# Kernel tuning notes

Measured on AMD Instinct MI355X. Metric: run time of the kernel, lower is better.

## Reference

```python
import jax, jax.numpy as jnp
import numpy as np

D_MODEL = 1024
D_HIDDEN = 32   # per-head MPS bond dimension
N_HEADS = 8
D_FF = 4096
EPS_LN = 1e-5
EPS_NORM = 1e-6


def layernorm(x, g, b):
    m = jnp.mean(x, axis=-1, keepdims=True)
    v = jnp.mean(jnp.square(x - m), axis=-1, keepdims=True)
    return (x - m) * jax.lax.rsqrt(v + EPS_LN) * g + b


def mps_recurrence(x, Wa, ba, h0, Wo, bo):
    # x: [B,S,D]. Per-token per-head transfer matrices A_t in R^{dh x dh}.
    B, S, D = x.shape
    A = (x @ Wa + ba).reshape(B, S, N_HEADS, D_HIDDEN, D_HIDDEN)
    A = jnp.moveaxis(A, 1, 0)  # [S,B,H,dh,dh]
    h_init = jnp.broadcast_to(h0, (B, N_HEADS, D_HIDDEN))  # [B,H,dh]

    def step(h, A_t):
        h = jnp.einsum('bhij,bhj->bhi', A_t, h)
        h = h / (jnp.linalg.norm(h, axis=-1, keepdims=True) + EPS_NORM)
        return h, h

    _, ys = jax.lax.scan(step, h_init, A)          # ys: [S,B,H,dh]
    ys = jnp.moveaxis(ys, 0, 1).reshape(B, S, N_HEADS * D_HIDDEN)
    return ys @ Wo + bo                            # [B,S,D]


def setup_inputs() -> dict:
    key = jax.random.key(0)
    ks = jax.random.split(key, 12)
    B, S, D = 4, 2048, D_MODEL
    inv = 1.0 / np.sqrt(D)
    inv_hd = 1.0 / np.sqrt(N_HEADS * D_HIDDEN)
    return {
        'x': jax.random.normal(ks[0], (B, S, D), jnp.float32),
        'ln1_g': jnp.ones((D,), jnp.float32),
        'ln1_b': jnp.zeros((D,), jnp.float32),
        'Wa': jax.random.normal(ks[1], (D, N_HEADS * D_HIDDEN * D_HIDDEN), jnp.float32) * inv,
        'ba': jnp.zeros((N_HEADS * D_HIDDEN * D_HIDDEN,), jnp.float32),
        'h0': jax.random.normal(ks[2], (N_HEADS, D_HIDDEN), jnp.float32) / np.sqrt(D_HIDDEN),
        'Wo': jax.random.normal(ks[3], (N_HEADS * D_HIDDEN, D), jnp.float32) * inv_hd,
        'bo': jnp.zeros((D,), jnp.float32),
        'ln2_g': jnp.ones((D,), jnp.float32),
        'ln2_b': jnp.zeros((D,), jnp.float32),
        'W1': jax.random.normal(ks[4], (D, D_FF), jnp.float32) * inv,
        'b1': jnp.zeros((D_FF,), jnp.float32),
        'W2': jax.random.normal(ks[5], (D_FF, D), jnp.float32) / np.sqrt(D_FF),
        'b2': jnp.zeros((D,), jnp.float32),
    }


def reference(x, ln1_g, ln1_b, Wa, ba, h0, Wo, bo, ln2_g, ln2_b, W1, b1, W2, b2):
    # Dropout in eval mode (identity).
    x = x + mps_recurrence(layernorm(x, ln1_g, ln1_b), Wa, ba, h0, Wo, bo)
    h = layernorm(x, ln2_g, ln2_b)
    ffn = jax.nn.gelu(h @ W1 + b1, approximate=False) @ W2 + b2
    return x + ffn
```

## Files before the change

### kernel.cpp

```cpp
#include <hip/hip_runtime.h>
#include <hip/hip_bf16.h>
#include <math.h>

typedef float f32x4 __attribute__((ext_vector_type(4)));
typedef __bf16 bf16x4 __attribute__((ext_vector_type(4)));
typedef __bf16 bf16x8 __attribute__((ext_vector_type(8)));

#define AS1(p) ((const __attribute__((address_space(1))) void*)(p))
#define AS3(p) ((__attribute__((address_space(3))) void*)(p))

static constexpr int D_MODEL = 1024;
static constexpr int S_LEN   = 2048;
static constexpr int BATCH   = 4;
static constexpr int NTOK    = BATCH * S_LEN;
static constexpr int NH      = 8;
static constexpr int DH      = 32;
static constexpr int NA      = NH * DH * DH;
static constexpr int D_FF    = 4096;
static constexpr int CHUNK   = 16;
static constexpr int NCHUNK  = S_LEN / CHUNK;

__device__ __forceinline__ void xcd_swizzle(int& bx, int& by) {
  int gx = gridDim.x;
  int nwg = gx * gridDim.y;
  int bid = by * gx + bx;
  int swz = (bid & 7) * (nwg >> 3) + (bid >> 3);
  bx = swz % gx;
  by = swz / gx;
}

__device__ __forceinline__ float gelu_erf_fast(float v) {
  float z = fabsf(v) * 0.70710678118654752f;
  float t = __builtin_amdgcn_rcpf(fmaf(0.3275911f, z, 1.0f));
  float p = t * (0.254829592f + t * (-0.284496736f + t * (1.421413741f +
            t * (-1.453152027f + t * 1.061405429f))));
  float e = __builtin_amdgcn_exp2f(-1.4426950408889634f * z * z);
  float er = 1.0f - p * e;
  er = (v < 0.0f) ? -er : er;
  return 0.5f * v * (1.0f + er);
}

__global__ __launch_bounds__(256) void transpose_bf16(
    const float* __restrict__ in, __bf16* __restrict__ out, int R, int C) {
  __shared__ float tile[32][33];
  int tx = threadIdx.x & 31, ty = threadIdx.x >> 5;
  int c0 = blockIdx.x * 32, r0 = blockIdx.y * 32;
  for (int i = ty; i < 32; i += 8)
    tile[i][tx] = in[(size_t)(r0 + i) * C + c0 + tx];
  __syncthreads();
  for (int i = ty; i < 32; i += 8)
    out[(size_t)(c0 + i) * R + r0 + tx] = (__bf16)tile[tx][i];
}

__global__ __launch_bounds__(256) void transpose_split(
    const float* __restrict__ in, __bf16* __restrict__ ohi,
    __bf16* __restrict__ olo, int R, int C) {
  __shared__ float tile[32][33];
  int tx = threadIdx.x & 31, ty = threadIdx.x >> 5;
  int c0 = blockIdx.x * 32, r0 = blockIdx.y * 32;
  for (int i = ty; i < 32; i += 8)
    tile[i][tx] = in[(size_t)(r0 + i) * C + c0 + tx];
  __syncthreads();
  for (int i = ty; i < 32; i += 8) {
    float v = tile[tx][i];
    __bf16 h = (__bf16)v;
    ohi[(size_t)(c0 + i) * R + r0 + tx] = h;
    olo[(size_t)(c0 + i) * R + r0 + tx] = (__bf16)(v - (float)h);
  }
}

template <int MODE>
__global__ __launch_bounds__(256) void ln_kernel(
    const float* __restrict__ in, const float* __restrict__ g,
    const float* __restrict__ bta, void* __restrict__ outv,
    void* __restrict__ outv2) {
  int row = blockIdx.x, tid = threadIdx.x;
  const float4* in4 = (const float4*)(in + (size_t)row * D_MODEL);
  float4 v = in4[tid];
  float s  = v.x + v.y + v.z + v.w;
  float ss = v.x * v.x + v.y * v.y + v.z * v.z + v.w * v.w;
  for (int o = 32; o; o >>= 1) { s += __shfl_down(s, o); ss += __shfl_down(ss, o); }
  __shared__ float ps[4], pq[4];
  int lane = tid & 63, w = tid >> 6;
  if (lane == 0) { ps[w] = s; pq[w] = ss; }
  __syncthreads();
  s  = ps[0] + ps[1] + ps[2] + ps[3];
  ss = pq[0] + pq[1] + pq[2] + pq[3];
  float mean = s * (1.0f / D_MODEL);
  float var  = ss * (1.0f / D_MODEL) - mean * mean;
  float inv  = rsqrtf(fmaxf(var, 0.0f) + 1e-5f);
  float4 gv = ((const float4*)g)[tid];
  float4 bv = ((const float4*)bta)[tid];
  float o0 = (v.x - mean) * inv * gv.x + bv.x;
  float o1 = (v.y - mean) * inv * gv.y + bv.y;
  float o2 = (v.z - mean) * inv * gv.z + bv.z;
  float o3 = (v.w - mean) * inv * gv.w + bv.w;
  if (MODE == 1) {
    float4 o = {o0, o1, o2, o3};
    ((float4*)outv)[(size_t)row * (D_MODEL / 4) + tid] = o;
  } else if (MODE == 0) {
    bf16x4 o;
    o[0] = (__bf16)o0; o[1] = (__bf16)o1; o[2] = (__bf16)o2; o[3] = (__bf16)o3;
    ((bf16x4*)outv)[(size_t)row * (D_MODEL / 4) + tid] = o;
  } else {
    bf16x4 oh, ol;
    oh[0] = (__bf16)o0; oh[1] = (__bf16)o1; oh[2] = (__bf16)o2; oh[3] = (__bf16)o3;
    ol[0] = (__bf16)(o0 - (float)oh[0]);
    ol[1] = (__bf16)(o1 - (float)oh[1]);
    ol[2] = (__bf16)(o2 - (float)oh[2]);
    ol[3] = (__bf16)(o3 - (float)oh[3]);
    ((bf16x4*)outv )[(size_t)row * (D_MODEL / 4) + tid] = oh;
    ((bf16x4*)outv2)[(size_t)row * (D_MODEL / 4) + tid] = ol;
  }
}

__global__ __launch_bounds__(256) void gemm_split_f32out(
    const __bf16* __restrict__ Ahi, const __bf16* __restrict__ Alo,
    const __bf16* __restrict__ BThi, const __bf16* __restrict__ BTlo,
    const float* __restrict__ bias, float* __restrict__ out,
    int M, int N, int K) {
  __shared__ __bf16 Ash[128 * 32], Asl[128 * 32];
  __shared__ __bf16 Bsh[128 * 32], Bsl[128 * 32];
  const int tid = threadIdx.x;
  const int lane = tid & 63, w = tid >> 6;
  int bx = blockIdx.x, by = blockIdx.y;
  xcd_swizzle(bx, by);
  const int m0 = by * 128, n0 = bx * 128;
  const int wm = (w >> 1) * 64, wn = (w & 1) * 64;

  f32x4 acc[4][4];
#pragma unroll
  for (int a = 0; a < 4; a++)
#pragma unroll
    for (int b = 0; b < 4; b++)
#pragma unroll
      for (int r = 0; r < 4; r++) acc[a][b][r] = 0.0f;

  const int srow = tid >> 2;
  const int soff = (tid & 3) * 16;
  const size_t goff0 = (size_t)(m0 + srow) * K + (soff >> 1);
  const size_t goff1 = (size_t)(m0 + srow + 64) * K + (soff >> 1);
  const size_t hoff0 = (size_t)(n0 + srow) * K + (soff >> 1);
  const size_t hoff1 = (size_t)(n0 + srow + 64) * K + (soff >> 1);
  const int l0 = srow * 64 + soff, l1 = (srow + 64) * 64 + soff;

  const int fm = lane & 15, fq = lane >> 4;
  for (int k0 = 0; k0 < K; k0 += 32) {
    __builtin_amdgcn_global_load_lds(AS1(Ahi + goff0 + k0), AS3((char*)Ash + l0), 16, 0, 0);
    __builtin_amdgcn_global_load_lds(AS1(Ahi + goff1 + k0), AS3((char*)Ash + l1), 16, 0, 0);
    __builtin_amdgcn_global_load_lds(AS1(Alo + goff0 + k0), AS3((char*)Asl + l0), 16, 0, 0);
    __builtin_amdgcn_global_load_lds(AS1(Alo + goff1 + k0), AS3((char*)Asl + l1), 16, 0, 0);
    __builtin_amdgcn_global_load_lds(AS1(BThi + hoff0 + k0), AS3((char*)Bsh + l0), 16, 0, 0);
    __builtin_amdgcn_global_load_lds(AS1(BThi + hoff1 + k0), AS3((char*)Bsh + l1), 16, 0, 0);
    __builtin_amdgcn_global_load_lds(AS1(BTlo + hoff0 + k0), AS3((char*)Bsl + l0), 16, 0, 0);
    __builtin_amdgcn_global_load_lds(AS1(BTlo + hoff1 + k0), AS3((char*)Bsl + l1), 16, 0, 0);
    __syncthreads();
    bf16x8 ah[4], al[4], bh[4], bl[4];
#pragma unroll
    for (int t = 0; t < 4; t++) {
      int o = (wm + t * 16 + fm) * 64 + fq * 16;
      ah[t] = *(const bf16x8*)((const char*)Ash + o);
      al[t] = *(const bf16x8*)((const char*)Asl + o);
    }
#pragma unroll
    for (int t = 0; t < 4; t++) {
      int o = (wn + t * 16 + fm) * 64 + fq * 16;
      bh[t] = *(const bf16x8*)((const char*)Bsh + o);
      bl[t] = *(const bf16x8*)((const char*)Bsl + o);
    }
#pragma unroll
    for (int tm = 0; tm < 4; tm++)
#pragma unroll
      for (int tn = 0; tn < 4; tn++) {
        acc[tm][tn] = __builtin_amdgcn_mfma_f32_16x16x32_bf16(ah[tm], bh[tn], acc[tm][tn], 0, 0, 0);
        acc[tm][tn] = __builtin_amdgcn_mfma_f32_16x16x32_bf16(ah[tm], bl[tn], acc[tm][tn], 0, 0, 0);
        acc[tm][tn] = __builtin_amdgcn_mfma_f32_16x16x32_bf16(al[tm], bh[tn], acc[tm][tn], 0, 0, 0);
      }
    __syncthreads();
  }

#pragma unroll
  for (int tn = 0; tn < 4; tn++) {
    int col = n0 + wn + tn * 16 + fm;
    float bv = bias[col];
#pragma unroll
    for (int tm = 0; tm < 4; tm++) {
#pragma unroll
      for (int r = 0; r < 4; r++) {
        int row = m0 + wm + tm * 16 + fq * 4 + r;
        out[(size_t)row * N + col] = acc[tm][tn][r] + bv;
      }
    }
  }
}

enum { EPI_BF16_BIAS = 0, EPI_BF16_BIAS_GELU = 1, EPI_F32_BIAS_RES = 2 };

template <int EPI>
__global__ __launch_bounds__(256) void gemm_bf16(
    const __bf16* __restrict__ Amat, const __bf16* __restrict__ BT,
    const float* __restrict__ bias, const float* __restrict__ res,
    void* __restrict__ out, int M, int N, int K) {
  __shared__ __bf16 smem[2 * 128 * 32];
  __bf16* As = smem;
  __bf16* Bs = smem + 128 * 32;
  const int tid = threadIdx.x;
  const int lane = tid & 63, w = tid >> 6;
  int bx = blockIdx.x, by = blockIdx.y;
  xcd_swizzle(bx, by);
  const int m0 = by * 128, n0 = bx * 128;
  const int wm = (w >> 1) * 64, wn = (w & 1) * 64;

  f32x4 acc[4][4];
#pragma unroll
  for (int a = 0; a < 4; a++)
#pragma unroll
    for (int b = 0; b < 4; b++)
#pragma unroll
      for (int r = 0; r < 4; r++) acc[a][b][r] = 0.0f;

  const int srow = tid >> 2;
  const int soff = (tid & 3) * 16;
  const __bf16* gA0 = Amat + (size_t)(m0 + srow) * K + (soff >> 1);
  const __bf16* gA1 = Amat + (size_t)(m0 + srow + 64) * K + (soff >> 1);
  const __bf16* gB0 = BT + (size_t)(n0 + srow) * K + (soff >> 1);
  const __bf16* gB1 = BT + (size_t)(n0 + srow + 64) * K + (soff >> 1);
  char* lA0 = (char*)As + srow * 64 + soff;
  char* lA1 = (char*)As + (srow + 64) * 64 + soff;
  char* lB0 = (char*)Bs + srow * 64 + soff;
  char* lB1 = (char*)Bs + (srow + 64) * 64 + soff;

  const int fm = lane & 15, fq = lane >> 4;
  for (int k0 = 0; k0 < K; k0 += 32) {
    __builtin_amdgcn_global_load_lds(AS1(gA0 + k0), AS3(lA0), 16, 0, 0);
    __builtin_amdgcn_global_load_lds(AS1(gA1 + k0), AS3(lA1), 16, 0, 0);
    __builtin_amdgcn_global_load_lds(AS1(gB0 + k0), AS3(lB0), 16, 0, 0);
    __builtin_amdgcn_global_load_lds(AS1(gB1 + k0), AS3(lB1), 16, 0, 0);
    __syncthreads();
    bf16x8 af[4], bf[4];
#pragma unroll
    for (int t = 0; t < 4; t++)
      af[t] = *(const bf16x8*)((const char*)As + (wm + t * 16 + fm) * 64 + fq * 16);
#pragma unroll
    for (int t = 0; t < 4; t++)
      bf[t] = *(const bf16x8*)((const char*)Bs + (wn + t * 16 + fm) * 64 + fq * 16);
#pragma unroll
    for (int tm = 0; tm < 4; tm++)
#pragma unroll
      for (int tn = 0; tn < 4; tn++)
        acc[tm][tn] = __builtin_amdgcn_mfma_f32_16x16x32_bf16(af[tm], bf[tn], acc[tm][tn], 0, 0, 0);
    __syncthreads();
  }

  if (EPI == EPI_BF16_BIAS_GELU) {
    float bvs[4];
#pragma unroll
    for (int tn = 0; tn < 4; tn++) bvs[tn] = bias[n0 + wn + tn * 16 + fm];
    char* patch = (char*)smem + w * 4096;
#pragma unroll
    for (int h2 = 0; h2 < 2; h2++) {
#pragma unroll
      for (int tmi = 0; tmi < 2; tmi++) {
        int tm = h2 * 2 + tmi;
#pragma unroll
        for (int tn = 0; tn < 4; tn++)
#pragma unroll
          for (int r = 0; r < 4; r++) {
            float vv = gelu_erf_fast(acc[tm][tn][r] + bvs[tn]);
            *(__bf16*)(patch + (tmi * 16 + fq * 4 + r) * 128 + (tn * 16 + fm) * 2) =
                (__bf16)vv;
          }
      }
      asm volatile("s_waitcnt lgkmcnt(0)" ::: "memory");
      int lrow = lane >> 3, lcb = (lane & 7) * 16;
#pragma unroll
      for (int rr = 0; rr < 4; rr++) {
        bf16x8 ov = *(const bf16x8*)(patch + (rr * 8 + lrow) * 128 + lcb);
        size_t grow = (size_t)(m0 + wm + h2 * 32 + rr * 8 + lrow);
        *(bf16x8*)((__bf16*)out + grow * N + n0 + wn + (lane & 7) * 8) = ov;
      }
      if (h2 == 0) asm volatile("s_waitcnt lgkmcnt(0)" ::: "memory");
    }
  } else {
#pragma unroll
    for (int tn = 0; tn < 4; tn++) {
      int col = n0 + wn + tn * 16 + fm;
      float bv = bias[col];
#pragma unroll
      for (int tm = 0; tm < 4; tm++) {
#pragma unroll
        for (int r = 0; r < 4; r++) {
          int row = m0 + wm + tm * 16 + fq * 4 + r;
          float v = acc[tm][tn][r] + bv;
          size_t idx = (size_t)row * N + col;
          if (EPI == EPI_F32_BIAS_RES) {
            ((float*)out)[idx] = v + res[idx];
          } else {
            ((__bf16*)out)[idx] = (__bf16)v;
          }
        }
      }
    }
  }
}

__global__ __launch_bounds__(64) void mps_chunkprod_f32(
    const float* __restrict__ A, float* __restrict__ P) {
  int bid = blockIdx.x;
  int c = bid & 127, hh = bid >> 7;
  int lane = threadIdx.x;
  int jj = lane & 31, half = lane >> 5;
  __shared__ float Albuf[2][DH * DH];

  float curc[32];
#pragma unroll
  for (int k = 0; k < 32; k++) curc[k] = (k == jj) ? 1.0f : 0.0f;

  const float* Abase = A + (size_t)(c * CHUNK) * NA + (size_t)hh * (DH * DH);

  {
    const float4* src = (const float4*)Abase;
    float4* dst = (float4*)Albuf[0];
#pragma unroll
    for (int r = 0; r < 4; r++) dst[lane + 64 * r] = src[lane + 64 * r];
  }
  __syncthreads();

  for (int t = 0; t < CHUNK; t++) {
    int cb = t & 1;
    float4 pf[4];
    if (t + 1 < CHUNK) {
      const float4* srcn = (const float4*)(Abase + (size_t)(t + 1) * NA);
#pragma unroll
      for (int r = 0; r < 4; r++) pf[r] = srcn[lane + 64 * r];
    }
    float nxt[16];
#pragma unroll
    for (int i16 = 0; i16 < 16; i16++) {
      const float4* ap = (const float4*)&Albuf[cb][(half * 16 + i16) * 32];
      float a0 = 0.f, a1 = 0.f, a2 = 0.f, a3 = 0.f;
#pragma unroll
      for (int k4 = 0; k4 < 8; k4++) {
        float4 av = ap[k4];
        a0 += av.x * curc[k4 * 4 + 0];
        a1 += av.y * curc[k4 * 4 + 1];
        a2 += av.z * curc[k4 * 4 + 2];
        a3 += av.w * curc[k4 * 4 + 3];
      }
      nxt[i16] = (a0 + a1) + (a2 + a3);
    }
#pragma unroll
    for (int i16 = 0; i16 < 16; i16++) {
      float mine  = nxt[i16];
      float other = __shfl_xor(mine, 32);
      curc[i16]      = (half == 0) ? mine  : other;
      curc[16 + i16] = (half == 0) ? other : mine;
    }
    if (t + 1 < CHUNK) {
      float4* dst = (float4*)Albuf[cb ^ 1];
#pragma unroll
      for (int r = 0; r < 4; r++) dst[lane + 64 * r] = pf[r];
      __syncthreads();
    }
  }

  float* Pc = P + (size_t)bid * (DH * DH);
#pragma unroll
  for (int k16 = 0; k16 < 16; k16++) {
    float v = (half == 0) ? curc[k16] : curc[16 + k16];
    Pc[(half * 16 + k16) * 32 + jj] = v;
  }
}

__global__ __launch_bounds__(64) void mps_chunkscan(
    const float* __restrict__ P, const float* __restrict__ h0,
    float* __restrict__ hstart) {
  int hh = blockIdx.x;
  int lane = threadIdx.x, i = lane & 31, half = lane >> 5;
  float hv = h0[hh * 32 + i];
  const float* row = P + (size_t)hh * NCHUNK * (DH * DH) + i * 32 + half * 16;
  int kb = half * 16;

  float4 pf0[4], pf1[4];
#pragma unroll
  for (int r = 0; r < 4; r++) pf0[r] = ((const float4*)row)[r];
#pragma unroll
  for (int r = 0; r < 4; r++) pf1[r] = ((const float4*)(row + DH * DH))[r];

  for (int c = 0; c < NCHUNK; c++) {
    if (lane < 32) hstart[((size_t)hh * NCHUNK + c) * 32 + i] = hv;
    float4 cur[4];
#pragma unroll
    for (int r = 0; r < 4; r++) cur[r] = pf0[r];
#pragma unroll
    for (int r = 0; r < 4; r++) pf0[r] = pf1[r];
    int cn = (c + 2 < NCHUNK) ? (c + 2) : (NCHUNK - 1);
#pragma unroll
    for (int r = 0; r < 4; r++)
      pf1[r] = ((const float4*)(row + (size_t)cn * (DH * DH)))[r];

    float a0 = 0.f, a1 = 0.f, a2 = 0.f, a3 = 0.f;
#pragma unroll
    for (int j4 = 0; j4 < 4; j4++) {
      float4 pv = cur[j4];
      a0 += pv.x * __shfl(hv, kb + j4 * 4 + 0);
      a1 += pv.y * __shfl(hv, kb + j4 * 4 + 1);
      a2 += pv.z * __shfl(hv, kb + j4 * 4 + 2);
      a3 += pv.w * __shfl(hv, kb + j4 * 4 + 3);
    }
    float y = (a0 + a1) + (a2 + a3);
    y += __shfl_xor(y, 32);
    float nn = y * y;
#pragma unroll
    for (int o = 16; o; o >>= 1) nn += __shfl_xor(nn, o);
    hv = y / (sqrtf(nn) + 1e-6f);
  }
}

__global__ __launch_bounds__(64) void mps_expand_f32(
    const float* __restrict__ A, const float* __restrict__ hstart,
    __bf16* __restrict__ ys, int tok0base) {
  int bid = blockIdx.x;
  int c = bid & 127, hh = bid >> 7;
  int lane = threadIdx.x, i = lane & 31, half = lane >> 5;
  float hv = hstart[(size_t)bid * 32 + i];
  const float* Ar = A + (size_t)(c * CHUNK) * NA + (size_t)hh * (DH * DH)
                    + i * 32 + half * 16;
  int kb = half * 16;

  float4 pf[4];
#pragma unroll
  for (int r = 0; r < 4; r++) pf[r] = ((const float4*)Ar)[r];

  for (int t = 0; t < CHUNK; t++) {
    float4 cur[4];
#pragma unroll
    for (int r = 0; r < 4; r++) cur[r] = pf[r];
    if (t + 1 < CHUNK) {
      const float4* an = (const float4*)(Ar + (size_t)(t + 1) * NA);
#pragma unroll
      for (int r = 0; r < 4; r++) pf[r] = an[r];
    }
    float a0 = 0.f, a1 = 0.f, a2 = 0.f, a3 = 0.f;
#pragma unroll
    for (int j4 = 0; j4 < 4; j4++) {
      float4 av = cur[j4];
      a0 += av.x * __shfl(hv, kb + j4 * 4 + 0);
      a1 += av.y * __shfl(hv, kb + j4 * 4 + 1);
      a2 += av.z * __shfl(hv, kb + j4 * 4 + 2);
      a3 += av.w * __shfl(hv, kb + j4 * 4 + 3);
    }
    float y = (a0 + a1) + (a2 + a3);
    y += __shfl_xor(y, 32);
    float nn = y * y;
#pragma unroll
    for (int o = 16; o; o >>= 1) nn += __shfl_xor(nn, o);
    hv = y / (sqrtf(nn) + 1e-6f);
    if (lane < 32)
      ys[(size_t)(tok0base + c * CHUNK + t) * (NH * DH) + hh * 32 + i] = (__bf16)hv;
  }
}

extern "C" void kernel_launch(void* const* d_in, const int* in_sizes, int n_in,
                              void* d_out, int out_size, void* d_ws, size_t ws_size,
                              hipStream_t stream) {
  const float* x     = (const float*)d_in[0];
  const float* ln1_g = (const float*)d_in[1];
  const float* ln1_b = (const float*)d_in[2];
  const float* Wa    = (const float*)d_in[3];
  const float* ba    = (const float*)d_in[4];
  const float* h0    = (const float*)d_in[5];
  const float* Wo    = (const float*)d_in[6];
  const float* bo    = (const float*)d_in[7];
  const float* ln2_g = (const float*)d_in[8];
  const float* ln2_b = (const float*)d_in[9];
  const float* W1    = (const float*)d_in[10];
  const float* b1    = (const float*)d_in[11];
  const float* W2    = (const float*)d_in[12];
  const float* b2    = (const float*)d_in[13];
  float* out = (float*)d_out;

  char* wsb = (char*)d_ws;
  size_t off = 0;
  auto alloc = [&](size_t bytes) -> void* {
    void* p = wsb + off;
    off += (bytes + 255) & ~(size_t)255;
    return p;
  };
  __bf16* WoT   = (__bf16*)alloc((size_t)(NH * DH) * D_MODEL * 2);
  __bf16* W1T   = (__bf16*)alloc((size_t)D_MODEL * D_FF * 2);
  __bf16* W2T   = (__bf16*)alloc((size_t)D_FF * D_MODEL * 2);
  __bf16* ys    = (__bf16*)alloc((size_t)NTOK * NH * DH * 2);
  float*  hst   = (float*) alloc((size_t)NH * NCHUNK * DH * 4);
  __bf16* xnh   = (__bf16*)alloc((size_t)NTOK * D_MODEL * 2);
  __bf16* xnl   = (__bf16*)alloc((size_t)NTOK * D_MODEL * 2);
  __bf16* WaTh  = (__bf16*)alloc((size_t)D_MODEL * NA * 2);
  __bf16* WaTl  = (__bf16*)alloc((size_t)D_MODEL * NA * 2);
  size_t tail0 = off;
  float*  Af32 = (float*) alloc((size_t)S_LEN * NA * 4);
  float*  P    = (float*) alloc((size_t)NH * NCHUNK * DH * DH * 4);
  __bf16* mid  = (__bf16*)(wsb + tail0);

  transpose_bf16<<<dim3(D_MODEL / 32, (NH * DH) / 32), 256, 0, stream>>>(Wo, WoT, NH * DH, D_MODEL);
  transpose_bf16<<<dim3(D_FF / 32, D_MODEL / 32), 256, 0, stream>>>(W1, W1T, D_MODEL, D_FF);
  transpose_bf16<<<dim3(D_MODEL / 32, D_FF / 32), 256, 0, stream>>>(W2, W2T, D_FF, D_MODEL);
  transpose_split<<<dim3(NA / 32, D_MODEL / 32), 256, 0, stream>>>(Wa, WaTh, WaTl, D_MODEL, NA);

  ln_kernel<2><<<NTOK, 256, 0, stream>>>(x, ln1_g, ln1_b, xnh, xnl);

  for (int b = 0; b < BATCH; b++) {
    gemm_split_f32out<<<dim3(NA / 128, S_LEN / 128), 256, 0, stream>>>(
        xnh + (size_t)b * S_LEN * D_MODEL, xnl + (size_t)b * S_LEN * D_MODEL,
        WaTh, WaTl, ba, Af32, S_LEN, NA, D_MODEL);
    mps_chunkprod_f32<<<NH * NCHUNK, 64, 0, stream>>>(Af32, P);
    mps_chunkscan<<<NH, 64, 0, stream>>>(P, h0, hst);
    mps_expand_f32<<<NH * NCHUNK, 64, 0, stream>>>(Af32, hst, ys, b * S_LEN);
  }

  gemm_bf16<EPI_F32_BIAS_RES><<<dim3(D_MODEL / 128, NTOK / 128), 256, 0, stream>>>(
      ys, WoT, bo, x, out, NTOK, D_MODEL, NH * DH);

  ln_kernel<0><<<NTOK, 256, 0, stream>>>(out, ln2_g, ln2_b, xnh, nullptr);

  gemm_bf16<EPI_BF16_BIAS_GELU><<<dim3(D_FF / 128, NTOK / 128), 256, 0, stream>>>(
      xnh, W1T, b1, nullptr, mid, NTOK, D_FF, D_MODEL);

  gemm_bf16<EPI_F32_BIAS_RES><<<dim3(D_MODEL / 128, NTOK / 128), 256, 0, stream>>>(
      mid, W2T, b2, out, out, NTOK, D_MODEL, D_FF);
}
```

Baseline: 1.565 ms.

## Store in-chunk prefix products and expand MPS states in parallel per token

The chunk-product kernel now writes each running prefix product of the transfer matrices back over A in place, and the scan reads the last prefix of each chunk instead of a separate P buffer. Each hidden state then becomes a single normalized matrix-vector product of a prefix with the chunk start state, using one wave per (token, head). This removes the 16-step serial dependency in the expand stage. The cost is an extra full write of the fp32 A buffer, and it relies on the per-step normalization being scale-invariant. The XCD swizzle for GEMM tiles is also changed so each XCD gets a contiguous group of column tiles.

```diff
diff --git a/kernel.cpp b/kernel.cpp
--- a/kernel.cpp
+++ b/kernel.cpp
@@ -21,12 +21,14 @@
 static constexpr int NCHUNK  = S_LEN / CHUNK;
 
 __device__ __forceinline__ void xcd_swizzle(int& bx, int& by) {
-  int gx = gridDim.x;
-  int nwg = gx * gridDim.y;
-  int bid = by * gx + bx;
-  int swz = (bid & 7) * (nwg >> 3) + (bid >> 3);
-  bx = swz % gx;
-  by = swz / gx;
+  int gx = gridDim.x, gy = gridDim.y;
+  int orig = by * gx + bx;
+  int xcd = orig & 7;
+  int q = orig >> 3;
+  int sx = gx >> 3;
+  int qh = q / gy;
+  bx = xcd * sx + qh;
+  by = q - qh * gy;
 }
 
 __device__ __forceinline__ float gelu_erf_fast(float v) {
@@ -305,7 +307,7 @@
 }
 
 __global__ __launch_bounds__(64) void mps_chunkprod_f32(
-    const float* __restrict__ A, float* __restrict__ P) {
+    float* __restrict__ A) {
   int bid = blockIdx.x;
   int c = bid & 127, hh = bid >> 7;
   int lane = threadIdx.x;
@@ -316,7 +318,7 @@
 #pragma unroll
   for (int k = 0; k < 32; k++) curc[k] = (k == jj) ? 1.0f : 0.0f;
 
-  const float* Abase = A + (size_t)(c * CHUNK) * NA + (size_t)hh * (DH * DH);
+  float* Abase = A + (size_t)(c * CHUNK) * NA + (size_t)hh * (DH * DH);
 
   {
     const float4* src = (const float4*)Abase;
@@ -349,6 +351,12 @@
       }
       nxt[i16] = (a0 + a1) + (a2 + a3);
     }
+    {
+      float* slot = Abase + (size_t)t * NA;
+#pragma unroll
+      for (int i16 = 0; i16 < 16; i16++)
+        slot[(half * 16 + i16) * 32 + jj] = nxt[i16];
+    }
 #pragma unroll
     for (int i16 = 0; i16 < 16; i16++) {
       float mine  = nxt[i16];
@@ -363,29 +371,24 @@
       __syncthreads();
     }
   }
-
-  float* Pc = P + (size_t)bid * (DH * DH);
-#pragma unroll
-  for (int k16 = 0; k16 < 16; k16++) {
-    float v = (half == 0) ? curc[k16] : curc[16 + k16];
-    Pc[(half * 16 + k16) * 32 + jj] = v;
-  }
 }
 
 __global__ __launch_bounds__(64) void mps_chunkscan(
-    const float* __restrict__ P, const float* __restrict__ h0,
+    const float* __restrict__ pref, const float* __restrict__ h0,
     float* __restrict__ hstart) {
   int hh = blockIdx.x;
   int lane = threadIdx.x, i = lane & 31, half = lane >> 5;
   float hv = h0[hh * 32 + i];
-  const float* row = P + (size_t)hh * NCHUNK * (DH * DH) + i * 32 + half * 16;
+  const size_t cstride = (size_t)CHUNK * NA;
+  const float* row = pref + (size_t)(CHUNK - 1) * NA + (size_t)hh * (DH * DH)
+                     + i * 32 + half * 16;
   int kb = half * 16;
 
   float4 pf0[4], pf1[4];
 #pragma unroll
   for (int r = 0; r < 4; r++) pf0[r] = ((const float4*)row)[r];
 #pragma unroll
-  for (int r = 0; r < 4; r++) pf1[r] = ((const float4*)(row + DH * DH))[r];
+  for (int r = 0; r < 4; r++) pf1[r] = ((const float4*)(row + cstride))[r];
 
   for (int c = 0; c < NCHUNK; c++) {
     if (lane < 32) hstart[((size_t)hh * NCHUNK + c) * 32 + i] = hv;
@@ -397,7 +400,7 @@
     int cn = (c + 2 < NCHUNK) ? (c + 2) : (NCHUNK - 1);
 #pragma unroll
     for (int r = 0; r < 4; r++)
-      pf1[r] = ((const float4*)(row + (size_t)cn * (DH * DH)))[r];
+      pf1[r] = ((const float4*)(row + (size_t)cn * cstride))[r];
 
     float a0 = 0.f, a1 = 0.f, a2 = 0.f, a3 = 0.f;
 #pragma unroll
@@ -417,48 +420,38 @@
   }
 }
 
-__global__ __launch_bounds__(64) void mps_expand_f32(
-    const float* __restrict__ A, const float* __restrict__ hstart,
+__global__ __launch_bounds__(256) void mps_expand_par(
+    const float* __restrict__ pref, const float* __restrict__ hstart,
     __bf16* __restrict__ ys, int tok0base) {
-  int bid = blockIdx.x;
-  int c = bid & 127, hh = bid >> 7;
-  int lane = threadIdx.x, i = lane & 31, half = lane >> 5;
-  float hv = hstart[(size_t)bid * 32 + i];
-  const float* Ar = A + (size_t)(c * CHUNK) * NA + (size_t)hh * (DH * DH)
-                    + i * 32 + half * 16;
+  int w = threadIdx.x >> 6, lane = threadIdx.x & 63;
+  int i = lane & 31, half = lane >> 5;
+  int task = blockIdx.x * 4 + w;
+  int hh = task & 7, tok = task >> 3;
+  int c = tok >> 4;
   int kb = half * 16;
 
-  float4 pf[4];
-#pragma unroll
-  for (int r = 0; r < 4; r++) pf[r] = ((const float4*)Ar)[r];
-
-  for (int t = 0; t < CHUNK; t++) {
-    float4 cur[4];
-#pragma unroll
-    for (int r = 0; r < 4; r++) cur[r] = pf[r];
-    if (t + 1 < CHUNK) {
-      const float4* an = (const float4*)(Ar + (size_t)(t + 1) * NA);
-#pragma unroll
-      for (int r = 0; r < 4; r++) pf[r] = an[r];
-    }
-    float a0 = 0.f, a1 = 0.f, a2 = 0.f, a3 = 0.f;
-#pragma unroll
-    for (int j4 = 0; j4 < 4; j4++) {
-      float4 av = cur[j4];
-      a0 += av.x * __shfl(hv, kb + j4 * 4 + 0);
-      a1 += av.y * __shfl(hv, kb + j4 * 4 + 1);
-      a2 += av.z * __shfl(hv, kb + j4 * 4 + 2);
-      a3 += av.w * __shfl(hv, kb + j4 * 4 + 3);
-    }
-    float y = (a0 + a1) + (a2 + a3);
-    y += __shfl_xor(y, 32);
-    float nn = y * y;
-#pragma unroll
-    for (int o = 16; o; o >>= 1) nn += __shfl_xor(nn, o);
-    hv = y / (sqrtf(nn) + 1e-6f);
-    if (lane < 32)
-      ys[(size_t)(tok0base + c * CHUNK + t) * (NH * DH) + hh * 32 + i] = (__bf16)hv;
-  }
+  float hv = hstart[((size_t)hh * NCHUNK + c) * 32 + i];
+  const float4* Mr = (const float4*)(pref + (size_t)tok * NA
+                     + (size_t)hh * (DH * DH) + i * 32 + half * 16);
+  float4 m0 = Mr[0], m1 = Mr[1], m2 = Mr[2], m3 = Mr[3];
+
+  float a0 = 0.f, a1 = 0.f, a2 = 0.f, a3 = 0.f;
+  a0 += m0.x * __shfl(hv, kb + 0);  a1 += m0.y * __shfl(hv, kb + 1);
+  a2 += m0.z * __shfl(hv, kb + 2);  a3 += m0.w * __shfl(hv, kb + 3);
+  a0 += m1.x * __shfl(hv, kb + 4);  a1 += m1.y * __shfl(hv, kb + 5);
+  a2 += m1.z * __shfl(hv, kb + 6);  a3 += m1.w * __shfl(hv, kb + 7);
+  a0 += m2.x * __shfl(hv, kb + 8);  a1 += m2.y * __shfl(hv, kb + 9);
+  a2 += m2.z * __shfl(hv, kb + 10); a3 += m2.w * __shfl(hv, kb + 11);
+  a0 += m3.x * __shfl(hv, kb + 12); a1 += m3.y * __shfl(hv, kb + 13);
+  a2 += m3.z * __shfl(hv, kb + 14); a3 += m3.w * __shfl(hv, kb + 15);
+  float y = (a0 + a1) + (a2 + a3);
+  y += __shfl_xor(y, 32);
+  float nn = y * y;
+#pragma unroll
+  for (int o = 16; o; o >>= 1) nn += __shfl_xor(nn, o);
+  float hvo = y / (sqrtf(nn) + 1e-6f);
+  if (lane < 32)
+    ys[(size_t)(tok0base + tok) * (NH * DH) + hh * 32 + i] = (__bf16)hvo;
 }
 
 extern "C" void kernel_launch(void* const* d_in, const int* in_sizes, int n_in,
@@ -498,7 +491,6 @@
   __bf16* WaTl  = (__bf16*)alloc((size_t)D_MODEL * NA * 2);
   size_t tail0 = off;
   float*  Af32 = (float*) alloc((size_t)S_LEN * NA * 4);
-  float*  P    = (float*) alloc((size_t)NH * NCHUNK * DH * DH * 4);
   __bf16* mid  = (__bf16*)(wsb + tail0);
 
   transpose_bf16<<<dim3(D_MODEL / 32, (NH * DH) / 32), 256, 0, stream>>>(Wo, WoT, NH * DH, D_MODEL);
@@ -512,9 +504,9 @@
     gemm_split_f32out<<<dim3(NA / 128, S_LEN / 128), 256, 0, stream>>>(
         xnh + (size_t)b * S_LEN * D_MODEL, xnl + (size_t)b * S_LEN * D_MODEL,
         WaTh, WaTl, ba, Af32, S_LEN, NA, D_MODEL);
-    mps_chunkprod_f32<<<NH * NCHUNK, 64, 0, stream>>>(Af32, P);
-    mps_chunkscan<<<NH, 64, 0, stream>>>(P, h0, hst);
-    mps_expand_f32<<<NH * NCHUNK, 64, 0, stream>>>(Af32, hst, ys, b * S_LEN);
+    mps_chunkprod_f32<<<NH * NCHUNK, 64, 0, stream>>>(Af32);
+    mps_chunkscan<<<NH, 64, 0, stream>>>(Af32, h0, hst);
+    mps_expand_par<<<(S_LEN * NH) / 4, 256, 0, stream>>>(Af32, hst, ys, b * S_LEN);
   }
 
   gemm_bf16<EPI_F32_BIAS_RES><<<dim3(D_MODEL / 128, NTOK / 128), 256, 0, stream>>>(
```

Result: slower. 1.620 ms (+3.5%).
